# Kernel tuning notes

Hardware: AMD Instinct MI355X
Metric: run time of the kernel (lower is better)

## Reference

```python
import jax, jax.numpy as jnp
import numpy as np
from jax import lax

B_, K_, T_, V_ = 2, 4, 1024, 1024
D_MODEL, EXPAND = 512, 2
D_INNER = EXPAND * D_MODEL          # 1024
N_STATE, D_CONV, DT_RANK, L_ = 16, 4, 32, 2


def setup_inputs() -> dict:
    key = jax.random.key(0)
    ks = jax.random.split(key, 9)
    s = 0.02
    A0 = jnp.log(jnp.arange(1, N_STATE + 1, dtype=jnp.float32))  # S4D-real init
    return {
        'codes': jax.random.randint(ks[0], (B_, K_, T_), 0, V_),
        'embed_w': jax.random.normal(ks[1], (K_, V_, D_MODEL), jnp.float32) * s,
        'norm_w': jnp.ones((L_, D_MODEL), jnp.float32),
        'in_proj_w': jax.random.normal(ks[2], (L_, 2 * D_INNER, D_MODEL), jnp.float32) * s,
        'conv_w': jax.random.normal(ks[3], (L_, D_INNER, 1, D_CONV), jnp.float32) * s,
        'conv_b': jnp.zeros((L_, D_INNER), jnp.float32),
        'x_proj_w': jax.random.normal(ks[4], (L_, DT_RANK + 2 * N_STATE, D_INNER), jnp.float32) * s,
        'dt_proj_w': jax.random.normal(ks[5], (L_, D_INNER, DT_RANK), jnp.float32) * s,
        'dt_proj_b': jnp.zeros((L_, D_INNER), jnp.float32),
        'A_log': jnp.broadcast_to(A0, (L_, D_INNER, N_STATE)) + 0.0,
        'D_skip': jnp.ones((L_, D_INNER), jnp.float32),
        'out_proj_w': jax.random.normal(ks[6], (L_, D_MODEL, D_INNER), jnp.float32) * s,
        'head_w': jax.random.normal(ks[7], (K_, D_MODEL, V_), jnp.float32) * s,
    }


def rmsnorm(x, w, eps=1e-6):
    return x * w * lax.rsqrt(jnp.mean(x * x, axis=-1, keepdims=True) + eps)


def causal_dwconv(x, w, b):
    # x: (B,T,D); w: (D,1,d_conv) depthwise; torch pads d_conv-1 both sides then slices [:T]
    # == left-pad-only causal conv.
    xt = x.transpose(0, 2, 1)  # (B,D,T)
    y = lax.conv_general_dilated(xt, w, (1,), [(D_CONV - 1, 0)],
                                 feature_group_count=D_INNER,
                                 dimension_numbers=('NCH', 'OIH', 'NCH'))
    return (y + b[None, :, None]).transpose(0, 2, 1)


def mamba_block(x, norm_w, in_w, cw, cb, xp_w, dtp_w, dtp_b, A_log, D_skip, out_w):
    res = x
    x = rmsnorm(x, norm_w)
    xz = x @ in_w.T                                   # (B,T,2*d_inner)
    x_ssm, z = jnp.split(xz, 2, axis=-1)
    x_ssm = jax.nn.silu(causal_dwconv(x_ssm, cw, cb))  # (B,T,D)
    x_dbl = x_ssm @ xp_w.T                            # (B,T,dt_rank+2N)
    dt_lr, Bm, Cm = jnp.split(x_dbl, [DT_RANK, DT_RANK + N_STATE], axis=-1)
    dt = jax.nn.softplus(dt_lr @ dtp_w.T + dtp_b)     # (B,T,D)
    A = -jnp.exp(A_log)                               # (D,N)
    dA = jnp.exp(dt[..., None] * A)                   # (B,T,D,N)
    dBx = dt[..., None] * Bm[:, :, None, :] * x_ssm[..., None]  # (B,T,D,N)

    def step(h, inp):
        dA_t, dBx_t, C_t = inp
        h = dA_t * h + dBx_t                          # (B,D,N)
        return h, jnp.einsum('bdn,bn->bd', h, C_t)

    h0 = jnp.zeros((x.shape[0], D_INNER, N_STATE), x.dtype)
    _, ys = lax.scan(step, h0, (dA.transpose(1, 0, 2, 3),
                                dBx.transpose(1, 0, 2, 3),
                                Cm.transpose(1, 0, 2)))
    y = ys.transpose(1, 0, 2) + x_ssm * D_skip        # (B,T,D)
    y = y * jax.nn.silu(z)
    return res + y @ out_w.T


def reference(codes, embed_w, norm_w, in_proj_w, conv_w, conv_b, x_proj_w,
              dt_proj_w, dt_proj_b, A_log, D_skip, out_proj_w, head_w):
    k_idx = jnp.arange(K_)[None, :, None]
    x = embed_w[k_idx, codes].sum(axis=1)             # (B,T,d_model): RVQ sum-embedding
    for l in range(L_):
        x = mamba_block(x, norm_w[l], in_proj_w[l], conv_w[l], conv_b[l],
                        x_proj_w[l], dt_proj_w[l], dt_proj_b[l],
                        A_log[l], D_skip[l], out_proj_w[l])
    return jnp.einsum('btd,kdv->bktv', x, head_w)     # (B,K,T,V)
```

## Files before the change

kernel.cpp:

```cpp
#include <hip/hip_runtime.h>
#include <hip/hip_bf16.h>


#define B_SZ 2
#define K_CB 4
#define T_SZ 1024
#define V_SZ 1024
#define DM 512
#define DI 1024
#define NS 16
#define DTR 32
#define NCHUNK 64
#define TCHUNK 16

typedef unsigned short u16;
typedef long long ll;
using short8 = __attribute__((ext_vector_type(8))) short;
using f32x4  = __attribute__((ext_vector_type(4))) float;

__device__ __forceinline__ float bf2f(u16 u) {
    union { unsigned int i; float f; } v; v.i = ((unsigned int)u) << 16; return v.f;
}
__device__ __forceinline__ u16 f2bf(float f) {
    union { float f; unsigned int i; } v; v.f = f;
    unsigned int x = v.i;
    return (u16)((x + 0x7fffu + ((x >> 16) & 1u)) >> 16);
}
__device__ __forceinline__ float siluf(float x) { return x / (1.f + __expf(-x)); }
__device__ __forceinline__ float softplusf(float x) { return (x > 20.f) ? x : log1pf(__expf(x)); }

__device__ __forceinline__ void gld16(const void* g, void* l) {
    __builtin_amdgcn_global_load_lds(
        (const __attribute__((address_space(1))) unsigned int*)g,
        (__attribute__((address_space(3))) unsigned int*)l, 16, 0, 0);
}

__global__ __launch_bounds__(256) void wcvt4_k(const float* __restrict__ in_w,
                                               const float* __restrict__ xp_w,
                                               const float* __restrict__ dtp_w,
                                               const float* __restrict__ out_w,
                                               u16* __restrict__ w_in, u16* __restrict__ w_xp,
                                               u16* __restrict__ w_dt, u16* __restrict__ w_out) {
    int i = (blockIdx.x * 256 + threadIdx.x) << 2;
    const float* s; u16* d;
    if (i < 2097152) { s = in_w + i; d = w_in + i; }
    else {
        i -= 2097152;
        if (i < 131072) { s = xp_w + i; d = w_xp + i; }
        else {
            i -= 131072;
            if (i < 65536) { s = dtp_w + i; d = w_dt + i; }
            else { i -= 65536; s = out_w + i; d = w_out + i; }
        }
    }
    float4 v = *(const float4*)s;
    ushort4 o; o.x = f2bf(v.x); o.y = f2bf(v.y); o.z = f2bf(v.z); o.w = f2bf(v.w);
    *(ushort4*)d = o;
}

__global__ __launch_bounds__(256) void ht_k(const float* __restrict__ w, u16* __restrict__ wt) {
    __shared__ float tile[64][65];
    int z = blockIdx.z;
    int v0 = blockIdx.x << 6, d0 = blockIdx.y << 6;
    int col = threadIdx.x & 63, rbase = threadIdx.x >> 6;
#pragma unroll
    for (int i = 0; i < 16; i++) {
        int row = (i << 2) + rbase;
        tile[row][col] = w[(ll)z * (DM * V_SZ) + (ll)(d0 + row) * V_SZ + v0 + col];
    }
    __syncthreads();
#pragma unroll
    for (int i = 0; i < 16; i++) {
        int vrow = (i << 2) + rbase;
        wt[(ll)z * (V_SZ * DM) + (ll)(v0 + vrow) * DM + d0 + col] = f2bf(tile[col][vrow]);
    }
}

__global__ __launch_bounds__(512) void embrms_k(const int* __restrict__ codes,
                                                const float* __restrict__ ew,
                                                const float* __restrict__ nw,
                                                float* __restrict__ x,
                                                u16* __restrict__ xn) {
    int row = blockIdx.x;
    int b = row >> 10, t = row & 1023;
    int d = threadIdx.x;
    float acc = 0.f;
#pragma unroll
    for (int k = 0; k < K_CB; k++) {
        int c = codes[b * (K_CB * T_SZ) + k * T_SZ + t];
        acc += ew[((ll)k * V_SZ + c) * DM + d];
    }
    x[(ll)row * DM + d] = acc;
    float ss = acc * acc;
#pragma unroll
    for (int off = 32; off > 0; off >>= 1) ss += __shfl_down(ss, off, 64);
    __shared__ float red[8];
    if ((d & 63) == 0) red[d >> 6] = ss;
    __syncthreads();
    float tot = red[0] + red[1] + red[2] + red[3] + red[4] + red[5] + red[6] + red[7];
    float scale = rsqrtf(tot * (1.0f / DM) + 1e-6f);
    xn[(ll)row * DM + d] = f2bf(acc * scale * nw[d]);
}

__global__ __launch_bounds__(256) void rmsnorm_k(const float* __restrict__ x,
                                                 const float* __restrict__ w,
                                                 u16* __restrict__ xn) {
    ll row = blockIdx.x;
    const float* xr = x + row * DM;
    int tid = threadIdx.x;
    float v0 = xr[tid], v1 = xr[tid + 256];
    float ss = v0 * v0 + v1 * v1;
#pragma unroll
    for (int off = 32; off > 0; off >>= 1) ss += __shfl_down(ss, off, 64);
    __shared__ float red[4];
    if ((tid & 63) == 0) red[tid >> 6] = ss;
    __syncthreads();
    float tot = red[0] + red[1] + red[2] + red[3];
    float scale = rsqrtf(tot * (1.0f / DM) + 1e-6f);
    xn[row * DM + tid]       = f2bf(v0 * scale * w[tid]);
    xn[row * DM + tid + 256] = f2bf(v1 * scale * w[tid + 256]);
}

template <int EP>
__global__ __launch_bounds__(256) void mgemm2_k(const u16* __restrict__ A, int lda,
                                                const u16* __restrict__ W,
                                                float* __restrict__ C,
                                                u16* __restrict__ Cb, int ldcb, int K) {
    __shared__ u16 As[4096];
    __shared__ u16 Bs[4096];
    int tid = threadIdx.x;
    int wave = tid >> 6, lane = tid & 63;
    int q = lane >> 4, r = lane & 15;
    int m0 = blockIdx.y << 7, n0 = blockIdx.x << 7;
    const u16* Wz = W;
    if (EP == 4) Wz += (ll)blockIdx.z * ((ll)V_SZ * DM);
    int wm = (wave >> 1) << 6, wn = (wave & 1) << 6;
    int sa0 = (wave << 7) + lane, sa1 = sa0 + 64;
    f32x4 acc[4][4];
#pragma unroll
    for (int i = 0; i < 4; i++)
#pragma unroll
        for (int j = 0; j < 4; j++) acc[i][j] = (f32x4){0.f, 0.f, 0.f, 0.f};

    for (int k0 = 0; k0 < K; k0 += 32) {
        gld16(A  + (ll)(m0 + (sa0 >> 2)) * lda + k0 + ((sa0 & 3) << 3), &As[wave << 10]);
        gld16(A  + (ll)(m0 + (sa1 >> 2)) * lda + k0 + ((sa1 & 3) << 3), &As[(wave << 10) + 512]);
        gld16(Wz + (ll)(n0 + (sa0 >> 2)) * K   + k0 + ((sa0 & 3) << 3), &Bs[wave << 10]);
        gld16(Wz + (ll)(n0 + (sa1 >> 2)) * K   + k0 + ((sa1 & 3) << 3), &Bs[(wave << 10) + 512]);
        __syncthreads();
        short8 af[4], bfr[4];
#pragma unroll
        for (int i = 0; i < 4; i++) af[i]  = *(const short8*)&As[((wm + (i << 4) + r) << 5) + (q << 3)];
#pragma unroll
        for (int j = 0; j < 4; j++) bfr[j] = *(const short8*)&Bs[((wn + (j << 4) + r) << 5) + (q << 3)];
#pragma unroll
        for (int i = 0; i < 4; i++)
#pragma unroll
            for (int j = 0; j < 4; j++)
                acc[i][j] = __builtin_amdgcn_mfma_f32_16x16x32_bf16(af[i], bfr[j], acc[i][j], 0, 0, 0);
        __syncthreads();
    }

#pragma unroll
    for (int i = 0; i < 4; i++)
#pragma unroll
        for (int j = 0; j < 4; j++)
#pragma unroll
            for (int g = 0; g < 4; g++) {
                int m = m0 + wm + (i << 4) + (q << 2) + g;
                int n = n0 + wn + (j << 4) + r;
                float v = acc[i][j][g];
                if (EP == 0) {
                    Cb[(ll)m * ldcb + n] = f2bf(v);
                } else {
                    int b = m >> 10, t = m & 1023;
                    C[(ll)b * (K_CB * (ll)T_SZ * V_SZ) + (ll)blockIdx.z * (T_SZ * V_SZ)
                      + (ll)t * V_SZ + n] = v;
                }
            }
}

template <int EP>
__global__ __launch_bounds__(256) void mgemm_k(const u16* __restrict__ A, int lda,
                                               const u16* __restrict__ W,
                                               float* __restrict__ C, int ldc, int K,
                                               const float* __restrict__ bias,
                                               u16* __restrict__ Cb, int ldcb) {
    __shared__ u16 As[64][40];
    __shared__ u16 Bs[64][40];
    int tid = threadIdx.x;
    int m0 = blockIdx.y << 6, n0 = blockIdx.x << 6;
    int lane = tid & 63, wave = tid >> 6;
    int q = lane >> 4, r = lane & 15;
    int wm = (wave >> 1) << 5, wn = (wave & 1) << 5;
    int srow = tid >> 2, sseg = (tid & 3) << 3;
    f32x4 acc[2][2];
#pragma unroll
    for (int i = 0; i < 2; i++)
#pragma unroll
        for (int j = 0; j < 2; j++) acc[i][j] = (f32x4){0.f, 0.f, 0.f, 0.f};

    for (int k0 = 0; k0 < K; k0 += 32) {
        *(uint4*)&As[srow][sseg] = *(const uint4*)&A[(ll)(m0 + srow) * lda + k0 + sseg];
        *(uint4*)&Bs[srow][sseg] = *(const uint4*)&W[(ll)(n0 + srow) * K + k0 + sseg];
        __syncthreads();
        short8 af[2], bfr[2];
#pragma unroll
        for (int i = 0; i < 2; i++) af[i]  = *(const short8*)&As[wm + (i << 4) + r][q << 3];
#pragma unroll
        for (int j = 0; j < 2; j++) bfr[j] = *(const short8*)&Bs[wn + (j << 4) + r][q << 3];
#pragma unroll
        for (int i = 0; i < 2; i++)
#pragma unroll
            for (int j = 0; j < 2; j++)
                acc[i][j] = __builtin_amdgcn_mfma_f32_16x16x32_bf16(af[i], bfr[j], acc[i][j], 0, 0, 0);
        __syncthreads();
    }

#pragma unroll
    for (int i = 0; i < 2; i++)
#pragma unroll
        for (int j = 0; j < 2; j++)
#pragma unroll
            for (int g = 0; g < 4; g++) {
                int m = m0 + wm + (i << 4) + (q << 2) + g;
                int n = n0 + wn + (j << 4) + r;
                float v = acc[i][j][g];
                if (EP == 1) {
                    C[(ll)m * ldc + n] = v;
                    Cb[(ll)m * ldcb + n] = f2bf(v);
                } else if (EP == 2) {
                    C[(ll)m * ldc + n] = softplusf(v + bias[n]);
                } else {
                    float nv = C[(ll)m * ldc + n] + v;
                    C[(ll)m * ldc + n] = nv;
                    Cb[(ll)m * ldcb + n] = f2bf(nv);
                }
            }
}

__global__ __launch_bounds__(256) void conv_k(const u16* __restrict__ xzb,
                                              const float* __restrict__ cw,
                                              const float* __restrict__ cb,
                                              float* __restrict__ xc,
                                              u16* __restrict__ xcb) {
    int row = blockIdx.x;
    int b = row >> 10, t = row & 1023;
    int c0 = threadIdx.x << 2;
    float4 a = *(const float4*)&cb[c0];
    float acc[4] = {a.x, a.y, a.z, a.w};
    float4 cwv[4];
#pragma unroll
    for (int e = 0; e < 4; e++) cwv[e] = *(const float4*)&cw[(c0 + e) << 2];
#pragma unroll
    for (int j = 0; j < 4; j++) {
        int tt = t - 3 + j;
        if (tt >= 0) {
            ushort4 v = *(const ushort4*)&xzb[((ll)(b * T_SZ + tt)) * (2 * DI) + c0];
            acc[0] = fmaf(bf2f(v.x), ((const float*)&cwv[0])[j], acc[0]);
            acc[1] = fmaf(bf2f(v.y), ((const float*)&cwv[1])[j], acc[1]);
            acc[2] = fmaf(bf2f(v.z), ((const float*)&cwv[2])[j], acc[2]);
            acc[3] = fmaf(bf2f(v.w), ((const float*)&cwv[3])[j], acc[3]);
        }
    }
    float4 s; ushort4 sb;
    s.x = siluf(acc[0]); s.y = siluf(acc[1]); s.z = siluf(acc[2]); s.w = siluf(acc[3]);
    sb.x = f2bf(s.x); sb.y = f2bf(s.y); sb.z = f2bf(s.z); sb.w = f2bf(s.w);
    *(float4*)&xc[(ll)row * DI + c0] = s;
    *(ushort4*)&xcb[(ll)row * DI + c0] = sb;
}

__global__ __launch_bounds__(256) void scan1_k(const float* __restrict__ dt,
                                               const float* __restrict__ xc,
                                               const float* __restrict__ xdbl,
                                               const float* __restrict__ A_log,
                                               float* __restrict__ pA, float* __restrict__ U) {
    int blk = blockIdx.x;
    int dblk = blk & 3;
    int c = (blk >> 2) & (NCHUNK - 1);
    int b = blk >> 8;
    int d = dblk * 256 + threadIdx.x;
    int t0 = c * TCHUNK;
    __shared__ float BC[TCHUNK][32];
    if (threadIdx.x < TCHUNK * 8) {
        int rr = threadIdx.x >> 3, cc = (threadIdx.x & 7) << 2;
        *(float4*)&BC[rr][cc] = *(const float4*)&xdbl[((ll)(b * T_SZ + t0 + rr)) * 64 + DTR + cc];
    }
    float Av[NS];
#pragma unroll
    for (int n4 = 0; n4 < 4; n4++) {
        float4 alv = *(const float4*)&A_log[d * NS + (n4 << 2)];
        Av[(n4 << 2) + 0] = -__expf(alv.x); Av[(n4 << 2) + 1] = -__expf(alv.y);
        Av[(n4 << 2) + 2] = -__expf(alv.z); Av[(n4 << 2) + 3] = -__expf(alv.w);
    }
    __syncthreads();
    float p[NS], u[NS];
#pragma unroll
    for (int n = 0; n < NS; n++) { p[n] = 1.f; u[n] = 0.f; }
#pragma unroll
    for (int s = 0; s < TCHUNK; s++) {
        ll ro = (ll)(b * T_SZ + t0 + s);
        float dtv = dt[ro * DI + d];
        float xv = xc[ro * DI + d];
        float dx = dtv * xv;
#pragma unroll
        for (int n = 0; n < NS; n++) {
            float a = __expf(dtv * Av[n]);
            p[n] *= a;
            u[n] = fmaf(a, u[n], dx * BC[s][n]);
        }
    }
    ll o = (((ll)b * NCHUNK + c) * DI + d) * NS;
#pragma unroll
    for (int n = 0; n < NS; n++) { pA[o + n] = p[n]; U[o + n] = u[n]; }
}

__global__ __launch_bounds__(256) void scan2_k(const float* __restrict__ pA,
                                               const float* __restrict__ U,
                                               float* __restrict__ hst) {
    int i = blockIdx.x * 256 + threadIdx.x;
    int b = i >> 14;
    int rest = i & 16383;
    float h = 0.f;
#pragma unroll
    for (int c = 0; c < NCHUNK; c++) {
        ll o = ((ll)b * NCHUNK + c) * (DI * NS) + rest;
        float pa = pA[o], u = U[o];
        hst[o] = h;
        h = fmaf(pa, h, u);
    }
}

__global__ __launch_bounds__(256) void scan3_k(const float* __restrict__ dt,
                                               const float* __restrict__ xc,
                                               const float* __restrict__ xdbl,
                                               const u16* __restrict__ xzb,
                                               const float* __restrict__ A_log,
                                               const float* __restrict__ Dk,
                                               const float* __restrict__ hst,
                                               u16* __restrict__ y) {
    int blk = blockIdx.x;
    int dblk = blk & 3;
    int c = (blk >> 2) & (NCHUNK - 1);
    int b = blk >> 8;
    int d = dblk * 256 + threadIdx.x;
    int t0 = c * TCHUNK;
    __shared__ float BC[TCHUNK][32];
    if (threadIdx.x < TCHUNK * 8) {
        int rr = threadIdx.x >> 3, cc = (threadIdx.x & 7) << 2;
        *(float4*)&BC[rr][cc] = *(const float4*)&xdbl[((ll)(b * T_SZ + t0 + rr)) * 64 + DTR + cc];
    }
    float Av[NS];
#pragma unroll
    for (int n4 = 0; n4 < 4; n4++) {
        float4 alv = *(const float4*)&A_log[d * NS + (n4 << 2)];
        Av[(n4 << 2) + 0] = -__expf(alv.x); Av[(n4 << 2) + 1] = -__expf(alv.y);
        Av[(n4 << 2) + 2] = -__expf(alv.z); Av[(n4 << 2) + 3] = -__expf(alv.w);
    }
    float h[NS];
    ll ho = (((ll)b * NCHUNK + c) * DI + d) * NS;
#pragma unroll
    for (int n = 0; n < NS; n++) h[n] = hst[ho + n];
    float Dv = Dk[d];
    __syncthreads();
#pragma unroll
    for (int s = 0; s < TCHUNK; s++) {
        ll ro = (ll)(b * T_SZ + t0 + s);
        float dtv = dt[ro * DI + d];
        float xv = xc[ro * DI + d];
        float dx = dtv * xv;
        float acc = 0.f;
#pragma unroll
        for (int n = 0; n < NS; n++) {
            float a = __expf(dtv * Av[n]);
            h[n] = fmaf(a, h[n], dx * BC[s][n]);
            acc = fmaf(h[n], BC[s][16 + n], acc);
        }
        float zv = bf2f(xzb[ro * (2 * DI) + DI + d]);
        y[ro * DI + d] = f2bf((acc + xv * Dv) * siluf(zv));
    }
}

extern "C" void kernel_launch(void* const* d_in, const int* in_sizes, int n_in,
                              void* d_out, int out_size, void* d_ws, size_t ws_size,
                              hipStream_t stream) {
    const int*   codes   = (const int*)d_in[0];
    const float* embed_w = (const float*)d_in[1];
    const float* norm_w  = (const float*)d_in[2];
    const float* in_w    = (const float*)d_in[3];
    const float* conv_w  = (const float*)d_in[4];
    const float* conv_b  = (const float*)d_in[5];
    const float* xp_w    = (const float*)d_in[6];
    const float* dtp_w   = (const float*)d_in[7];
    const float* dtp_b   = (const float*)d_in[8];
    const float* A_log   = (const float*)d_in[9];
    const float* D_skip  = (const float*)d_in[10];
    const float* out_w   = (const float*)d_in[11];
    const float* head_w  = (const float*)d_in[12];
    float* out = (float*)d_out;

    float* ws = (float*)d_ws;
    float* x    = ws;
    float* xc   = x + 1048576;
    float* dtb  = xc + 2097152;
    float* xdbl = dtb + 2097152;
    float* pA   = xdbl + 131072;
    float* Uh   = pA + 2097152;

    u16* us       = (u16*)(Uh + 2097152);
    u16* xz_bf    = us;
    u16* xc_bf    = xz_bf + 4194304;
    u16* ybxn_bf  = xc_bf + 2097152;
    u16* xdbl_bf  = ybxn_bf + 2097152;
    u16* w_in_bf  = xdbl_bf + 131072;
    u16* w_xp_bf  = w_in_bf + 2097152;
    u16* w_dt_bf  = w_xp_bf + 131072;
    u16* w_out_bf = w_dt_bf + 65536;
    u16* w_hd_bf  = w_out_bf + 1048576;

    u16* xn_bf = ybxn_bf;
    u16* y_bf  = ybxn_bf;
    u16* x_bf  = xc_bf;

    const int M = B_SZ * T_SZ;

    wcvt4_k<<<3264, 256, 0, stream>>>(in_w, xp_w, dtp_w, out_w,
                                      w_in_bf, w_xp_bf, w_dt_bf, w_out_bf);
    ht_k<<<dim3(16, 8, 4), 256, 0, stream>>>(head_w, w_hd_bf);

    embrms_k<<<M, 512, 0, stream>>>(codes, embed_w, norm_w, x, xn_bf);

    for (int l = 0; l < 2; l++) {
        const float* al = A_log + l * DI * NS;
        if (l == 1)
            rmsnorm_k<<<M, 256, 0, stream>>>(x, norm_w + DM, xn_bf);
        mgemm2_k<0><<<dim3(16, 16), 256, 0, stream>>>(xn_bf, DM, w_in_bf + l * 1048576,
                                                      nullptr, xz_bf, 2 * DI, DM);
        conv_k<<<M, 256, 0, stream>>>(xz_bf, conv_w + l * DI * 4, conv_b + l * DI, xc, xc_bf);
        mgemm_k<1><<<dim3(1, 32), 256, 0, stream>>>(xc_bf, DI, w_xp_bf + l * 65536,
                                                    xdbl, 64, DI, nullptr, xdbl_bf, 64);
        mgemm_k<2><<<dim3(16, 32), 256, 0, stream>>>(xdbl_bf, 64, w_dt_bf + l * 32768,
                                                     dtb, DI, DTR, dtp_b + l * DI, nullptr, 0);
        scan1_k<<<512, 256, 0, stream>>>(dtb, xc, xdbl, al, pA, Uh);
        scan2_k<<<128, 256, 0, stream>>>(pA, Uh, Uh);
        scan3_k<<<512, 256, 0, stream>>>(dtb, xc, xdbl, xz_bf, al, D_skip + l * DI, Uh, y_bf);
        mgemm_k<3><<<dim3(8, 32), 256, 0, stream>>>(y_bf, DI, w_out_bf + l * 524288,
                                                    x, DM, DI, nullptr, x_bf, DM);
    }

    mgemm2_k<4><<<dim3(8, 16, 4), 256, 0, stream>>>(x_bf, DM, w_hd_bf,
                                                    out, nullptr, 0, DM);
}
```

Measured before the change: 334.0 us.

## Fuse setup kernels, inline dt projection into scans, use narrower GEMM tiles

Result: slower. 357.7 us (+7.1%).

```diff
diff --git a/kernel.cpp b/kernel.cpp
--- a/kernel.cpp
+++ b/kernel.cpp
@@ -35,71 +35,72 @@
         (__attribute__((address_space(3))) unsigned int*)l, 16, 0, 0);
 }
 
-__global__ __launch_bounds__(256) void wcvt4_k(const float* __restrict__ in_w,
+__global__ __launch_bounds__(256) void mega0_k(const float* __restrict__ in_w,
                                                const float* __restrict__ xp_w,
-                                               const float* __restrict__ dtp_w,
                                                const float* __restrict__ out_w,
                                                u16* __restrict__ w_in, u16* __restrict__ w_xp,
-                                               u16* __restrict__ w_dt, u16* __restrict__ w_out) {
-    int i = (blockIdx.x * 256 + threadIdx.x) << 2;
-    const float* s; u16* d;
-    if (i < 2097152) { s = in_w + i; d = w_in + i; }
-    else {
-        i -= 2097152;
-        if (i < 131072) { s = xp_w + i; d = w_xp + i; }
+                                               u16* __restrict__ w_out,
+                                               const float* __restrict__ head_w,
+                                               u16* __restrict__ w_hd,
+                                               const int* __restrict__ codes,
+                                               const float* __restrict__ ew,
+                                               const float* __restrict__ nw,
+                                               float* __restrict__ x,
+                                               u16* __restrict__ xn) {
+    __shared__ float tile[64][65];
+    int bid = blockIdx.x;
+    int tid = threadIdx.x;
+    if (bid < 3200) {
+        int i = (bid * 256 + tid) << 2;
+        const float* s; u16* d;
+        if (i < 2097152) { s = in_w + i; d = w_in + i; }
         else {
-            i -= 131072;
-            if (i < 65536) { s = dtp_w + i; d = w_dt + i; }
-            else { i -= 65536; s = out_w + i; d = w_out + i; }
-        }
-    }
-    float4 v = *(const float4*)s;
-    ushort4 o; o.x = f2bf(v.x); o.y = f2bf(v.y); o.z = f2bf(v.z); o.w = f2bf(v.w);
-    *(ushort4*)d = o;
-}
-
-__global__ __launch_bounds__(256) void ht_k(const float* __restrict__ w, u16* __restrict__ wt) {
-    __shared__ float tile[64][65];
-    int z = blockIdx.z;
-    int v0 = blockIdx.x << 6, d0 = blockIdx.y << 6;
-    int col = threadIdx.x & 63, rbase = threadIdx.x >> 6;
-#pragma unroll
-    for (int i = 0; i < 16; i++) {
-        int row = (i << 2) + rbase;
-        tile[row][col] = w[(ll)z * (DM * V_SZ) + (ll)(d0 + row) * V_SZ + v0 + col];
-    }
-    __syncthreads();
-#pragma unroll
-    for (int i = 0; i < 16; i++) {
-        int vrow = (i << 2) + rbase;
-        wt[(ll)z * (V_SZ * DM) + (ll)(v0 + vrow) * DM + d0 + col] = f2bf(tile[col][vrow]);
-    }
-}
-
-__global__ __launch_bounds__(512) void embrms_k(const int* __restrict__ codes,
-                                                const float* __restrict__ ew,
-                                                const float* __restrict__ nw,
-                                                float* __restrict__ x,
-                                                u16* __restrict__ xn) {
-    int row = blockIdx.x;
-    int b = row >> 10, t = row & 1023;
-    int d = threadIdx.x;
-    float acc = 0.f;
-#pragma unroll
-    for (int k = 0; k < K_CB; k++) {
-        int c = codes[b * (K_CB * T_SZ) + k * T_SZ + t];
-        acc += ew[((ll)k * V_SZ + c) * DM + d];
-    }
-    x[(ll)row * DM + d] = acc;
-    float ss = acc * acc;
-#pragma unroll
-    for (int off = 32; off > 0; off >>= 1) ss += __shfl_down(ss, off, 64);
-    __shared__ float red[8];
-    if ((d & 63) == 0) red[d >> 6] = ss;
-    __syncthreads();
-    float tot = red[0] + red[1] + red[2] + red[3] + red[4] + red[5] + red[6] + red[7];
-    float scale = rsqrtf(tot * (1.0f / DM) + 1e-6f);
-    xn[(ll)row * DM + d] = f2bf(acc * scale * nw[d]);
+            i -= 2097152;
+            if (i < 131072) { s = xp_w + i; d = w_xp + i; }
+            else { i -= 131072; s = out_w + i; d = w_out + i; }
+        }
+        float4 v = *(const float4*)s;
+        ushort4 o; o.x = f2bf(v.x); o.y = f2bf(v.y); o.z = f2bf(v.z); o.w = f2bf(v.w);
+        *(ushort4*)d = o;
+    } else if (bid < 3712) {
+        int idx = bid - 3200;
+        int z = idx >> 7, rest = idx & 127;
+        int d0 = (rest >> 4) << 6, v0 = (rest & 15) << 6;
+        int col = tid & 63, rbase = tid >> 6;
+#pragma unroll
+        for (int i = 0; i < 16; i++) {
+            int row = (i << 2) + rbase;
+            tile[row][col] = head_w[(ll)z * (DM * V_SZ) + (ll)(d0 + row) * V_SZ + v0 + col];
+        }
+        __syncthreads();
+#pragma unroll
+        for (int i = 0; i < 16; i++) {
+            int vrow = (i << 2) + rbase;
+            w_hd[(ll)z * (V_SZ * DM) + (ll)(v0 + vrow) * DM + d0 + col] = f2bf(tile[col][vrow]);
+        }
+    } else {
+        int row = bid - 3712;
+        int b = row >> 10, t = row & 1023;
+        float a0 = 0.f, a1 = 0.f;
+#pragma unroll
+        for (int k = 0; k < K_CB; k++) {
+            int c = codes[b * (K_CB * T_SZ) + k * T_SZ + t];
+            a0 += ew[((ll)k * V_SZ + c) * DM + tid];
+            a1 += ew[((ll)k * V_SZ + c) * DM + tid + 256];
+        }
+        x[(ll)row * DM + tid]       = a0;
+        x[(ll)row * DM + tid + 256] = a1;
+        float ss = a0 * a0 + a1 * a1;
+#pragma unroll
+        for (int off = 32; off > 0; off >>= 1) ss += __shfl_down(ss, off, 64);
+        float* red = &tile[0][0];
+        if ((tid & 63) == 0) red[tid >> 6] = ss;
+        __syncthreads();
+        float tot = red[0] + red[1] + red[2] + red[3];
+        float scale = rsqrtf(tot * (1.0f / DM) + 1e-6f);
+        xn[(ll)row * DM + tid]       = f2bf(a0 * scale * nw[tid]);
+        xn[(ll)row * DM + tid + 256] = f2bf(a1 * scale * nw[tid + 256]);
+    }
 }
 
 __global__ __launch_bounds__(256) void rmsnorm_k(const float* __restrict__ x,
@@ -122,41 +123,39 @@
 }
 
 template <int EP>
-__global__ __launch_bounds__(256) void mgemm2_k(const u16* __restrict__ A, int lda,
+__global__ __launch_bounds__(256) void mgemm3_k(const u16* __restrict__ A, int lda,
                                                 const u16* __restrict__ W,
                                                 float* __restrict__ C,
                                                 u16* __restrict__ Cb, int ldcb, int K) {
     __shared__ u16 As[4096];
-    __shared__ u16 Bs[4096];
+    __shared__ u16 Bs[2048];
     int tid = threadIdx.x;
     int wave = tid >> 6, lane = tid & 63;
     int q = lane >> 4, r = lane & 15;
-    int m0 = blockIdx.y << 7, n0 = blockIdx.x << 7;
-    const u16* Wz = W;
-    if (EP == 4) Wz += (ll)blockIdx.z * ((ll)V_SZ * DM);
-    int wm = (wave >> 1) << 6, wn = (wave & 1) << 6;
-    int sa0 = (wave << 7) + lane, sa1 = sa0 + 64;
-    f32x4 acc[4][4];
+    int m0 = blockIdx.y << 7, n0 = blockIdx.x << 6;
+    int wm = (wave >> 1) << 6, wn = (wave & 1) << 5;
+    int sA0 = (wave << 7) + lane, sA1 = sA0 + 64;
+    int sB = (wave << 6) + lane;
+    f32x4 acc[4][2];
 #pragma unroll
     for (int i = 0; i < 4; i++)
 #pragma unroll
-        for (int j = 0; j < 4; j++) acc[i][j] = (f32x4){0.f, 0.f, 0.f, 0.f};
+        for (int j = 0; j < 2; j++) acc[i][j] = (f32x4){0.f, 0.f, 0.f, 0.f};
 
     for (int k0 = 0; k0 < K; k0 += 32) {
-        gld16(A  + (ll)(m0 + (sa0 >> 2)) * lda + k0 + ((sa0 & 3) << 3), &As[wave << 10]);
-        gld16(A  + (ll)(m0 + (sa1 >> 2)) * lda + k0 + ((sa1 & 3) << 3), &As[(wave << 10) + 512]);
-        gld16(Wz + (ll)(n0 + (sa0 >> 2)) * K   + k0 + ((sa0 & 3) << 3), &Bs[wave << 10]);
-        gld16(Wz + (ll)(n0 + (sa1 >> 2)) * K   + k0 + ((sa1 & 3) << 3), &Bs[(wave << 10) + 512]);
-        __syncthreads();
-        short8 af[4], bfr[4];
+        gld16(A + (ll)(m0 + (sA0 >> 2)) * lda + k0 + ((sA0 & 3) << 3), &As[wave << 10]);
+        gld16(A + (ll)(m0 + (sA1 >> 2)) * lda + k0 + ((sA1 & 3) << 3), &As[(wave << 10) + 512]);
+        gld16(W + (ll)(n0 + (sB  >> 2)) * K   + k0 + ((sB  & 3) << 3), &Bs[wave << 9]);
+        __syncthreads();
+        short8 af[4], bfr[2];
 #pragma unroll
         for (int i = 0; i < 4; i++) af[i]  = *(const short8*)&As[((wm + (i << 4) + r) << 5) + (q << 3)];
 #pragma unroll
-        for (int j = 0; j < 4; j++) bfr[j] = *(const short8*)&Bs[((wn + (j << 4) + r) << 5) + (q << 3)];
+        for (int j = 0; j < 2; j++) bfr[j] = *(const short8*)&Bs[((wn + (j << 4) + r) << 5) + (q << 3)];
 #pragma unroll
         for (int i = 0; i < 4; i++)
 #pragma unroll
-            for (int j = 0; j < 4; j++)
+            for (int j = 0; j < 2; j++)
                 acc[i][j] = __builtin_amdgcn_mfma_f32_16x16x32_bf16(af[i], bfr[j], acc[i][j], 0, 0, 0);
         __syncthreads();
     }
@@ -164,7 +163,7 @@
 #pragma unroll
     for (int i = 0; i < 4; i++)
 #pragma unroll
-        for (int j = 0; j < 4; j++)
+        for (int j = 0; j < 2; j++)
 #pragma unroll
             for (int g = 0; g < 4; g++) {
                 int m = m0 + wm + (i << 4) + (q << 2) + g;
@@ -173,9 +172,9 @@
                 if (EP == 0) {
                     Cb[(ll)m * ldcb + n] = f2bf(v);
                 } else {
+                    int z = n >> 10, vv = n & 1023;
                     int b = m >> 10, t = m & 1023;
-                    C[(ll)b * (K_CB * (ll)T_SZ * V_SZ) + (ll)blockIdx.z * (T_SZ * V_SZ)
-                      + (ll)t * V_SZ + n] = v;
+                    C[((ll)(b * K_CB + z) * T_SZ + t) * V_SZ + vv] = v;
                 }
             }
 }
@@ -184,7 +183,6 @@
 __global__ __launch_bounds__(256) void mgemm_k(const u16* __restrict__ A, int lda,
                                                const u16* __restrict__ W,
                                                float* __restrict__ C, int ldc, int K,
-                                               const float* __restrict__ bias,
                                                u16* __restrict__ Cb, int ldcb) {
     __shared__ u16 As[64][40];
     __shared__ u16 Bs[64][40];
@@ -228,9 +226,6 @@
                 float v = acc[i][j][g];
                 if (EP == 1) {
                     C[(ll)m * ldc + n] = v;
-                    Cb[(ll)m * ldcb + n] = f2bf(v);
-                } else if (EP == 2) {
-                    C[(ll)m * ldc + n] = softplusf(v + bias[n]);
                 } else {
                     float nv = C[(ll)m * ldc + n] + v;
                     C[(ll)m * ldc + n] = nv;
@@ -270,9 +265,10 @@
     *(ushort4*)&xcb[(ll)row * DI + c0] = sb;
 }
 
-__global__ __launch_bounds__(256) void scan1_k(const float* __restrict__ dt,
-                                               const float* __restrict__ xc,
+__global__ __launch_bounds__(256) void scan1_k(const float* __restrict__ xc,
                                                const float* __restrict__ xdbl,
+                                               const float* __restrict__ dtw,
+                                               const float* __restrict__ dtb_,
                                                const float* __restrict__ A_log,
                                                float* __restrict__ pA, float* __restrict__ U) {
     int blk = blockIdx.x;
@@ -281,11 +277,19 @@
     int b = blk >> 8;
     int d = dblk * 256 + threadIdx.x;
     int t0 = c * TCHUNK;
-    __shared__ float BC[TCHUNK][32];
-    if (threadIdx.x < TCHUNK * 8) {
-        int rr = threadIdx.x >> 3, cc = (threadIdx.x & 7) << 2;
-        *(float4*)&BC[rr][cc] = *(const float4*)&xdbl[((ll)(b * T_SZ + t0 + rr)) * 64 + DTR + cc];
-    }
+    __shared__ float BC[TCHUNK][64];
+    {
+        int rr = threadIdx.x >> 4, cc = (threadIdx.x & 15) << 2;
+        *(float4*)&BC[rr][cc] = *(const float4*)&xdbl[((ll)(b * T_SZ + t0 + rr)) * 64 + cc];
+    }
+    float wd[DTR];
+#pragma unroll
+    for (int k4 = 0; k4 < 8; k4++) {
+        float4 w4 = *(const float4*)&dtw[d * DTR + (k4 << 2)];
+        wd[(k4 << 2) + 0] = w4.x; wd[(k4 << 2) + 1] = w4.y;
+        wd[(k4 << 2) + 2] = w4.z; wd[(k4 << 2) + 3] = w4.w;
+    }
+    float bias = dtb_[d];
     float Av[NS];
 #pragma unroll
     for (int n4 = 0; n4 < 4; n4++) {
@@ -300,14 +304,17 @@
 #pragma unroll
     for (int s = 0; s < TCHUNK; s++) {
         ll ro = (ll)(b * T_SZ + t0 + s);
-        float dtv = dt[ro * DI + d];
+        float adt = bias;
+#pragma unroll
+        for (int k = 0; k < DTR; k++) adt = fmaf(BC[s][k], wd[k], adt);
+        float dtv = softplusf(adt);
         float xv = xc[ro * DI + d];
         float dx = dtv * xv;
 #pragma unroll
         for (int n = 0; n < NS; n++) {
-            float a = __expf(dtv * Av[n]);
-            p[n] *= a;
-            u[n] = fmaf(a, u[n], dx * BC[s][n]);
+            float aa = __expf(dtv * Av[n]);
+            p[n] *= aa;
+            u[n] = fmaf(aa, u[n], dx * BC[s][DTR + n]);
         }
     }
     ll o = (((ll)b * NCHUNK + c) * DI + d) * NS;
@@ -331,10 +338,11 @@
     }
 }
 
-__global__ __launch_bounds__(256) void scan3_k(const float* __restrict__ dt,
-                                               const float* __restrict__ xc,
+__global__ __launch_bounds__(256) void scan3_k(const float* __restrict__ xc,
                                                const float* __restrict__ xdbl,
                                                const u16* __restrict__ xzb,
+                                               const float* __restrict__ dtw,
+                                               const float* __restrict__ dtb_,
                                                const float* __restrict__ A_log,
                                                const float* __restrict__ Dk,
                                                const float* __restrict__ hst,
@@ -345,11 +353,19 @@
     int b = blk >> 8;
     int d = dblk * 256 + threadIdx.x;
     int t0 = c * TCHUNK;
-    __shared__ float BC[TCHUNK][32];
-    if (threadIdx.x < TCHUNK * 8) {
-        int rr = threadIdx.x >> 3, cc = (threadIdx.x & 7) << 2;
-        *(float4*)&BC[rr][cc] = *(const float4*)&xdbl[((ll)(b * T_SZ + t0 + rr)) * 64 + DTR + cc];
-    }
+    __shared__ float BC[TCHUNK][64];
+    {
+        int rr = threadIdx.x >> 4, cc = (threadIdx.x & 15) << 2;
+        *(float4*)&BC[rr][cc] = *(const float4*)&xdbl[((ll)(b * T_SZ + t0 + rr)) * 64 + cc];
+    }
+    float wd[DTR];
+#pragma unroll
+    for (int k4 = 0; k4 < 8; k4++) {
+        float4 w4 = *(const float4*)&dtw[d * DTR + (k4 << 2)];
+        wd[(k4 << 2) + 0] = w4.x; wd[(k4 << 2) + 1] = w4.y;
+        wd[(k4 << 2) + 2] = w4.z; wd[(k4 << 2) + 3] = w4.w;
+    }
+    float bias = dtb_[d];
     float Av[NS];
 #pragma unroll
     for (int n4 = 0; n4 < 4; n4++) {
@@ -366,15 +382,18 @@
 #pragma unroll
     for (int s = 0; s < TCHUNK; s++) {
         ll ro = (ll)(b * T_SZ + t0 + s);
-        float dtv = dt[ro * DI + d];
+        float adt = bias;
+#pragma unroll
+        for (int k = 0; k < DTR; k++) adt = fmaf(BC[s][k], wd[k], adt);
+        float dtv = softplusf(adt);
         float xv = xc[ro * DI + d];
         float dx = dtv * xv;
         float acc = 0.f;
 #pragma unroll
         for (int n = 0; n < NS; n++) {
-            float a = __expf(dtv * Av[n]);
-            h[n] = fmaf(a, h[n], dx * BC[s][n]);
-            acc = fmaf(h[n], BC[s][16 + n], acc);
+            float aa = __expf(dtv * Av[n]);
+            h[n] = fmaf(aa, h[n], dx * BC[s][DTR + n]);
+            acc = fmaf(h[n], BC[s][DTR + NS + n], acc);
         }
         float zv = bf2f(xzb[ro * (2 * DI) + DI + d]);
         y[ro * DI + d] = f2bf((acc + xv * Dv) * siluf(zv));
@@ -402,8 +421,7 @@
     float* ws = (float*)d_ws;
     float* x    = ws;
     float* xc   = x + 1048576;
-    float* dtb  = xc + 2097152;
-    float* xdbl = dtb + 2097152;
+    float* xdbl = xc + 2097152;
     float* pA   = xdbl + 131072;
     float* Uh   = pA + 2097152;
 
@@ -411,43 +429,34 @@
     u16* xz_bf    = us;
     u16* xc_bf    = xz_bf + 4194304;
     u16* ybxn_bf  = xc_bf + 2097152;
-    u16* xdbl_bf  = ybxn_bf + 2097152;
-    u16* w_in_bf  = xdbl_bf + 131072;
+    u16* w_in_bf  = ybxn_bf + 2097152;
     u16* w_xp_bf  = w_in_bf + 2097152;
-    u16* w_dt_bf  = w_xp_bf + 131072;
-    u16* w_out_bf = w_dt_bf + 65536;
+    u16* w_out_bf = w_xp_bf + 131072;
     u16* w_hd_bf  = w_out_bf + 1048576;
 
     u16* xn_bf = ybxn_bf;
     u16* y_bf  = ybxn_bf;
     u16* x_bf  = xc_bf;
 
-    const int M = B_SZ * T_SZ;
-
-    wcvt4_k<<<3264, 256, 0, stream>>>(in_w, xp_w, dtp_w, out_w,
-                                      w_in_bf, w_xp_bf, w_dt_bf, w_out_bf);
-    ht_k<<<dim3(16, 8, 4), 256, 0, stream>>>(head_w, w_hd_bf);
-
-    embrms_k<<<M, 512, 0, stream>>>(codes, embed_w, norm_w, x, xn_bf);
+    mega0_k<<<5760, 256, 0, stream>>>(in_w, xp_w, out_w, w_in_bf, w_xp_bf, w_out_bf,
+                                      head_w, w_hd_bf, codes, embed_w, norm_w, x, xn_bf);
 
     for (int l = 0; l < 2; l++) {
-        const float* al = A_log + l * DI * NS;
         if (l == 1)
-            rmsnorm_k<<<M, 256, 0, stream>>>(x, norm_w + DM, xn_bf);
-        mgemm2_k<0><<<dim3(16, 16), 256, 0, stream>>>(xn_bf, DM, w_in_bf + l * 1048576,
+            rmsnorm_k<<<2048, 256, 0, stream>>>(x, norm_w + DM, xn_bf);
+        mgemm3_k<0><<<dim3(32, 16), 256, 0, stream>>>(xn_bf, DM, w_in_bf + l * 1048576,
                                                       nullptr, xz_bf, 2 * DI, DM);
-        conv_k<<<M, 256, 0, stream>>>(xz_bf, conv_w + l * DI * 4, conv_b + l * DI, xc, xc_bf);
+        conv_k<<<2048, 256, 0, stream>>>(xz_bf, conv_w + l * DI * 4, conv_b + l * DI, xc, xc_bf);
         mgemm_k<1><<<dim3(1, 32), 256, 0, stream>>>(xc_bf, DI, w_xp_bf + l * 65536,
-                                                    xdbl, 64, DI, nullptr, xdbl_bf, 64);
-        mgemm_k<2><<<dim3(16, 32), 256, 0, stream>>>(xdbl_bf, 64, w_dt_bf + l * 32768,
-                                                     dtb, DI, DTR, dtp_b + l * DI, nullptr, 0);
-        scan1_k<<<512, 256, 0, stream>>>(dtb, xc, xdbl, al, pA, Uh);
+                                                    xdbl, 64, DI, nullptr, 0);
+        scan1_k<<<512, 256, 0, stream>>>(xc, xdbl, dtp_w + l * DI * DTR, dtp_b + l * DI,
+                                         A_log + l * DI * NS, pA, Uh);
         scan2_k<<<128, 256, 0, stream>>>(pA, Uh, Uh);
-        scan3_k<<<512, 256, 0, stream>>>(dtb, xc, xdbl, xz_bf, al, D_skip + l * DI, Uh, y_bf);
+        scan3_k<<<512, 256, 0, stream>>>(xc, xdbl, xz_bf, dtp_w + l * DI * DTR, dtp_b + l * DI,
+                                         A_log + l * DI * NS, D_skip + l * DI, Uh, y_bf);
         mgemm_k<3><<<dim3(8, 32), 256, 0, stream>>>(y_bf, DI, w_out_bf + l * 524288,
-                                                    x, DM, DI, nullptr, x_bf, DM);
-    }
-
-    mgemm2_k<4><<<dim3(8, 16, 4), 256, 0, stream>>>(x_bf, DM, w_hd_bf,
-                                                    out, nullptr, 0, DM);
-}
+                                                    x, DM, DI, x_bf, DM);
+    }
+
+    mgemm3_k<4><<<dim3(64, 16), 256, 0, stream>>>(x_bf, DM, w_hd_bf, out, nullptr, 0, DM);
+}
```
